# Kernel optimization log

Measured on AMD Instinct MI355X. Metric: run time of the kernel, lower is better.

The kernel has to match this reference:

```python
import jax, jax.numpy as jnp
import numpy as np

B, N, G = 16, 6000, 512
NUM_PAD_GT = 64  # zero-padded gt rows per image


def _make_boxes(key, shape):
    # sample two corner points and sort so (y1,x1) <= (y2,x2)
    r = jax.random.uniform(key, shape[:-1] + (4,), dtype=jnp.float32)
    lo = jnp.minimum(r[..., :2], r[..., 2:])
    hi = jnp.maximum(r[..., :2], r[..., 2:])
    return jnp.concatenate([lo, hi], axis=-1)


def setup_inputs() -> dict:
    key = jax.random.key(0)
    k1, k2, k3 = jax.random.split(key, 3)
    rois = _make_boxes(k1, (B, N, 4))
    gt_boxes = _make_boxes(k2, (B, G, 4))
    # zero-pad tail gt rows (remove_zero_padding signal)
    gt_boxes = gt_boxes.at[:, G - NUM_PAD_GT:, :].set(0.0)
    # ids in [-2, 18]: <0 crowd, ==0 padding, >0 real classes
    gt_ids = jax.random.randint(k3, (B, G), 0, 21, dtype=jnp.int64) - 2
    gt_ids = jnp.where(jnp.arange(G) >= G - NUM_PAD_GT, 0, gt_ids)
    return {"rois": rois, "gt_ids": gt_ids, "gt_boxes": gt_boxes}


def _pairwise_iou(boxes1, boxes2):
    # boxes1: [B,N,4], boxes2: [B,G,4] in (y1,x1,y2,x2) -> IoU [B,N,G]
    b1 = boxes1[:, :, None, :]  # [B,N,1,4]
    b2 = boxes2[:, None, :, :]  # [B,1,G,4]
    y1 = jnp.maximum(b1[..., 0], b2[..., 0])
    x1 = jnp.maximum(b1[..., 1], b2[..., 1])
    y2 = jnp.minimum(b1[..., 2], b2[..., 2])
    x2 = jnp.minimum(b1[..., 3], b2[..., 3])
    inter = jnp.maximum(y2 - y1, 0.0) * jnp.maximum(x2 - x1, 0.0)
    area1 = (b1[..., 2] - b1[..., 0]) * (b1[..., 3] - b1[..., 1])
    area2 = (b2[..., 2] - b2[..., 0]) * (b2[..., 3] - b2[..., 1])
    union = area1 + area2 - inter
    return inter / (union + 1e-8)


def reference(rois, gt_ids, gt_boxes):
    # remove_zero_padding -> validity masks (jit-friendly: mask instead of gather)
    valid_roi = jnp.sum(jnp.abs(rois), axis=-1) > 0.0      # [B,N]
    valid_gt = jnp.sum(jnp.abs(gt_boxes), axis=-1) > 0.0   # [B,G]
    crowd = valid_gt & (gt_ids < 0)                          # [B,G]
    non_crowd = valid_gt & (gt_ids > 0)                      # [B,G]

    iou = _pairwise_iou(rois, gt_boxes)                      # [B,N,G]
    # max IoU against non-crowd / crowd gt subsets (masked cols -> 0, IoU >= 0)
    iou_nc_max = jnp.max(jnp.where(non_crowd[:, None, :], iou, 0.0), axis=2)
    iou_c_max = jnp.max(jnp.where(crowd[:, None, :], iou, 0.0), axis=2)
    iou_nc_max = jnp.where(valid_roi, iou_nc_max, 0.0)       # [B,N]
    iou_c_max = jnp.where(valid_roi, iou_c_max, 0.0)

    positive_mask = valid_roi & (iou_nc_max >= 0.5)
    negative_mask = valid_roi & (iou_nc_max < 0.5) & (iou_c_max < 1e-3)

    iou_maxes = jnp.stack([iou_nc_max, iou_c_max], axis=1)   # [B,2,N]
    return iou_maxes, positive_mask, negative_mask
```

## Files before the change

### kernel.cpp

```cpp
#include <hip/hip_runtime.h>

#define BB 16
#define NN 6000
#define GG 512
#define WAVES 8
#define RPT 2
#define RPB (RPT * 64)

__device__ __forceinline__ int rfl(int v) { return __builtin_amdgcn_readfirstlane(v); }

__global__ __launch_bounds__(64 * WAVES, 8) void det_kernel(
    const float4* __restrict__ rois,
    const int*    __restrict__ gt_ids,
    const float4* __restrict__ gt_boxes,
    float*        __restrict__ out)
{
    __shared__ float4 s_box[GG];
    __shared__ float4 s_area4[GG / 4];
    __shared__ float  s_ncm[WAVES][RPB];
    __shared__ float  s_cm[WAVES][RPB];
    __shared__ int    s_wn[WAVES], s_wc[WAVES];
    float* s_area = (float*)s_area4;

    const int b    = blockIdx.y;
    const int tid  = threadIdx.x;
    const int wave = tid >> 6;
    const int lane = tid & 63;

    const int nbase = blockIdx.x * RPB;
    float4 r[RPT];
    float  rs[RPT];
    #pragma unroll
    for (int i = 0; i < RPT; ++i) {
        int n = nbase + i * 64 + lane;
        r[i] = (n < NN) ? rois[b * NN + n] : make_float4(0.f, 0.f, 0.f, 0.f);
    }
    const float4 box = gt_boxes[b * GG + tid];
    const int    id  = gt_ids[b * GG + tid];

    #pragma unroll
    for (int i = 0; i < RPT; ++i)
        rs[i] = (r[i].z - r[i].x) * (r[i].w - r[i].y) + 1e-8f;

    const float asum = fabsf(box.x) + fabsf(box.y) + fabsf(box.z) + fabsf(box.w);
    const bool pn = (asum > 0.0f) && (id > 0);
    const bool pc = (asum > 0.0f) && (id < 0);
    const unsigned long long mn = __ballot(pn);
    const unsigned long long mc = __ballot(pc);
    if (lane == 0) { s_wn[wave] = __popcll(mn); s_wc[wave] = __popcll(mc); }
    __syncthreads();

    int bn = 0, bc = 0, ncnt = 0, ccnt = 0;
    #pragma unroll
    for (int w = 0; w < WAVES; ++w) {
        int pw = s_wn[w], cw = s_wc[w];
        if (w < wave) { bn += pw; bc += cw; }
        ncnt += pw; ccnt += cw;
    }
    const int lo = GG - ccnt;
    int nc_eff = (ncnt + 3) & ~3;
    int lo_pad = lo & ~3;
    if (nc_eff > lo_pad) nc_eff = lo_pad;

    {
        const unsigned long long lt = (1ULL << lane) - 1ULL;
        if (pn) {
            int idx = bn + __popcll(mn & lt);
            s_box[idx]  = box;
            s_area[idx] = (box.z - box.x) * (box.w - box.y);
        }
        if (pc) {
            int idx = (GG - 1) - (bc + __popcll(mc & lt));
            s_box[idx]  = box;
            s_area[idx] = (box.z - box.x) * (box.w - box.y);
        }
        const float4 z = make_float4(0.f, 0.f, 0.f, 0.f);
        if (tid < 4) {
            int i = ncnt + tid;
            if (i < nc_eff) { s_box[i] = z; s_area[i] = 0.f; }
        } else if (tid < 8) {
            int i = lo_pad + (tid - 4);
            if (i < lo) { s_box[i] = z; s_area[i] = 0.f; }
        }
    }
    __syncthreads();

    auto tval = [](const float4& rr, float rsum, const float4& g4, float ga) -> float {
        float dy = fminf(rr.z, g4.z) - fmaxf(rr.x, g4.x);
        float dx = fminf(rr.w, g4.w) - fmaxf(rr.y, g4.y);
        float inter = fmaxf(fmaxf(dy, 0.f) * dx, 0.f);
        return inter * __builtin_amdgcn_rcpf(rsum + ga);
    };

    float anc[RPT] = {0.f, 0.f};
    float ac[RPT]  = {0.f, 0.f};

    auto run = [&](int q0, int q1, float* acc) {
        if (q0 >= q1) return;
        float4 nb0 = s_box[4 * q0 + 0];
        float4 nb1 = s_box[4 * q0 + 1];
        float4 nb2 = s_box[4 * q0 + 2];
        float4 nb3 = s_box[4 * q0 + 3];
        float4 na  = s_area4[q0];
        #pragma unroll 2
        for (int q = q0; q < q1; ++q) {
            const float4 cb0 = nb0, cb1 = nb1, cb2 = nb2, cb3 = nb3, ca = na;
            const int qn = (q + 1 < q1) ? q + 1 : q0;
            nb0 = s_box[4 * qn + 0];
            nb1 = s_box[4 * qn + 1];
            nb2 = s_box[4 * qn + 2];
            nb3 = s_box[4 * qn + 3];
            na  = s_area4[qn];
            #pragma unroll
            for (int i = 0; i < RPT; ++i) {
                float t0 = tval(r[i], rs[i], cb0, ca.x);
                float t1 = tval(r[i], rs[i], cb1, ca.y);
                float t2 = tval(r[i], rs[i], cb2, ca.z);
                float t3 = tval(r[i], rs[i], cb3, ca.w);
                acc[i] = fmaxf(acc[i], fmaxf(fmaxf(t0, t1), fmaxf(t2, t3)));
            }
        }
    };

    {
        const int ngr = nc_eff >> 2;
        const int gpw = (ngr + WAVES - 1) / WAVES;
        const int q0 = rfl(wave * gpw);
        const int q1 = rfl(min(ngr, q0 + gpw));
        run(q0, q1, anc);
    }
    {
        const int cg0 = lo_pad >> 2;
        const int cgn = (GG >> 2) - cg0;
        const int gpw = (cgn + WAVES - 1) / WAVES;
        const int q0 = rfl(cg0 + wave * gpw);
        const int q1 = rfl(min(GG >> 2, q0 + gpw));
        run(q0, q1, ac);
    }

    #pragma unroll
    for (int i = 0; i < RPT; ++i) {
        s_ncm[wave][i * 64 + lane] = anc[i];
        s_cm[wave][i * 64 + lane]  = ac[i];
    }
    __syncthreads();

    if (tid < RPB) {
        const int n = nbase + tid;
        if (n < NN) {
            float a = s_ncm[0][tid], c = s_cm[0][tid];
            #pragma unroll
            for (int w = 1; w < WAVES; ++w) {
                a = fmaxf(a, s_ncm[w][tid]);
                c = fmaxf(c, s_cm[w][tid]);
            }
            const float4 rr = (tid < 64) ? r[0] : r[1];
            const float vr =
                ((fabsf(rr.x) + fabsf(rr.y) + fabsf(rr.z) + fabsf(rr.w)) > 0.f) ? 1.f : 0.f;
            a *= vr;
            c *= vr;
            const float nc_max = a * __builtin_amdgcn_rcpf(1.f - a);
            const float c_max  = c * __builtin_amdgcn_rcpf(1.f - c);

            out[b * 2 * NN + n]      = nc_max;
            out[b * 2 * NN + NN + n] = c_max;
            const float pos = (vr > 0.f && nc_max >= 0.5f) ? 1.0f : 0.0f;
            const float neg = (vr > 0.f && nc_max < 0.5f && c_max < 0.001f) ? 1.0f : 0.0f;
            out[BB * 2 * NN + b * NN + n]           = pos;
            out[BB * 2 * NN + BB * NN + b * NN + n] = neg;
        }
    }
}

extern "C" void kernel_launch(void* const* d_in, const int* in_sizes, int n_in,
                              void* d_out, int out_size, void* d_ws, size_t ws_size,
                              hipStream_t stream) {
    const float4* rois     = (const float4*)d_in[0];
    const int*    gt_ids   = (const int*)d_in[1];
    const float4* gt_boxes = (const float4*)d_in[2];
    float*        out      = (float*)d_out;

    dim3 grid((NN + RPB - 1) / RPB, BB);
    det_kernel<<<grid, 64 * WAVES, 0, stream>>>(rois, gt_ids, gt_boxes, out);
}
```

Measured before the change: 25.08 us.

## Process three ROIs per lane with packed float2 math and inline gt areas

Raises the ROIs per thread from two to three, so each LDS-loaded gt box is reused across more ROIs and the grid shrinks. Two of the ROIs are computed with float2 operations, which may map to packed FP32 instructions, and the third is handled as a scalar. The separate gt area array in LDS is removed and each area is recomputed in the loop. ROI validity is staged through shared memory. The occupancy hint is dropped from launch bounds, so register pressure and occupancy can change, and with 6000 not divisible by 192 the last block has more idle lanes.

```diff
diff --git a/kernel.cpp b/kernel.cpp
--- a/kernel.cpp
+++ b/kernel.cpp
@@ -4,23 +4,24 @@
 #define NN 6000
 #define GG 512
 #define WAVES 8
-#define RPT 2
+#define RPT 3
 #define RPB (RPT * 64)
 
 __device__ __forceinline__ int rfl(int v) { return __builtin_amdgcn_readfirstlane(v); }
-
-__global__ __launch_bounds__(64 * WAVES, 8) void det_kernel(
+__device__ __forceinline__ float2 min2s(float2 a, float s) { return make_float2(fminf(a.x, s), fminf(a.y, s)); }
+__device__ __forceinline__ float2 max2s(float2 a, float s) { return make_float2(fmaxf(a.x, s), fmaxf(a.y, s)); }
+
+__global__ __launch_bounds__(64 * WAVES) void det_kernel(
     const float4* __restrict__ rois,
     const int*    __restrict__ gt_ids,
     const float4* __restrict__ gt_boxes,
     float*        __restrict__ out)
 {
     __shared__ float4 s_box[GG];
-    __shared__ float4 s_area4[GG / 4];
     __shared__ float  s_ncm[WAVES][RPB];
     __shared__ float  s_cm[WAVES][RPB];
+    __shared__ float  s_val[RPB];
     __shared__ int    s_wn[WAVES], s_wc[WAVES];
-    float* s_area = (float*)s_area4;
 
     const int b    = blockIdx.y;
     const int tid  = threadIdx.x;
@@ -29,7 +30,6 @@
 
     const int nbase = blockIdx.x * RPB;
     float4 r[RPT];
-    float  rs[RPT];
     #pragma unroll
     for (int i = 0; i < RPT; ++i) {
         int n = nbase + i * 64 + lane;
@@ -38,9 +38,14 @@
     const float4 box = gt_boxes[b * GG + tid];
     const int    id  = gt_ids[b * GG + tid];
 
+    float rsv[RPT];
     #pragma unroll
-    for (int i = 0; i < RPT; ++i)
-        rs[i] = (r[i].z - r[i].x) * (r[i].w - r[i].y) + 1e-8f;
+    for (int i = 0; i < RPT; ++i) {
+        rsv[i] = (r[i].z - r[i].x) * (r[i].w - r[i].y) + 1e-8f;
+        if (wave == 0)
+            s_val[i * 64 + lane] =
+                ((fabsf(r[i].x) + fabsf(r[i].y) + fabsf(r[i].z) + fabsf(r[i].w)) > 0.f) ? 1.f : 0.f;
+    }
 
     const float asum = fabsf(box.x) + fabsf(box.y) + fabsf(box.z) + fabsf(box.w);
     const bool pn = (asum > 0.0f) && (id > 0);
@@ -64,61 +69,74 @@
 
     {
         const unsigned long long lt = (1ULL << lane) - 1ULL;
-        if (pn) {
-            int idx = bn + __popcll(mn & lt);
-            s_box[idx]  = box;
-            s_area[idx] = (box.z - box.x) * (box.w - box.y);
-        }
-        if (pc) {
-            int idx = (GG - 1) - (bc + __popcll(mc & lt));
-            s_box[idx]  = box;
-            s_area[idx] = (box.z - box.x) * (box.w - box.y);
-        }
+        if (pn) s_box[bn + __popcll(mn & lt)] = box;
+        if (pc) s_box[(GG - 1) - (bc + __popcll(mc & lt))] = box;
         const float4 z = make_float4(0.f, 0.f, 0.f, 0.f);
         if (tid < 4) {
             int i = ncnt + tid;
-            if (i < nc_eff) { s_box[i] = z; s_area[i] = 0.f; }
+            if (i < nc_eff) s_box[i] = z;
         } else if (tid < 8) {
             int i = lo_pad + (tid - 4);
-            if (i < lo) { s_box[i] = z; s_area[i] = 0.f; }
+            if (i < lo) s_box[i] = z;
         }
     }
     __syncthreads();
 
-    auto tval = [](const float4& rr, float rsum, const float4& g4, float ga) -> float {
-        float dy = fminf(rr.z, g4.z) - fmaxf(rr.x, g4.x);
-        float dx = fminf(rr.w, g4.w) - fmaxf(rr.y, g4.y);
-        float inter = fmaxf(fmaxf(dy, 0.f) * dx, 0.f);
-        return inter * __builtin_amdgcn_rcpf(rsum + ga);
+    const float2 ry1c = make_float2(r[0].x, r[1].x);
+    const float2 rx1c = make_float2(r[0].y, r[1].y);
+    const float2 ry2c = make_float2(r[0].z, r[1].z);
+    const float2 rx2c = make_float2(r[0].w, r[1].w);
+    const float2 rs01 = make_float2(rsv[0], rsv[1]);
+    const float4 r2   = r[2];
+    const float  rs2  = rsv[2];
+
+    auto tduo = [&](const float4& g4, float ga) -> float2 {
+        float2 dy = min2s(ry2c, g4.z) - max2s(ry1c, g4.x);
+        float2 dx = min2s(rx2c, g4.w) - max2s(rx1c, g4.y);
+        float2 p  = max2s(dy, 0.f) * dx;
+        float2 it = max2s(p, 0.f);
+        return make_float2(it.x * __builtin_amdgcn_rcpf(rs01.x + ga),
+                           it.y * __builtin_amdgcn_rcpf(rs01.y + ga));
     };
-
-    float anc[RPT] = {0.f, 0.f};
-    float ac[RPT]  = {0.f, 0.f};
-
-    auto run = [&](int q0, int q1, float* acc) {
+    auto tsc = [&](const float4& g4, float ga) -> float {
+        float dy = fminf(r2.z, g4.z) - fmaxf(r2.x, g4.x);
+        float dx = fminf(r2.w, g4.w) - fmaxf(r2.y, g4.y);
+        float it = fmaxf(fmaxf(dy, 0.f) * dx, 0.f);
+        return it * __builtin_amdgcn_rcpf(rs2 + ga);
+    };
+
+    float2 a01n = make_float2(0.f, 0.f), a01c = make_float2(0.f, 0.f);
+    float  a2n = 0.f, a2c = 0.f;
+
+    auto run = [&](int q0, int q1, float2& acc2, float& acc1) {
         if (q0 >= q1) return;
         float4 nb0 = s_box[4 * q0 + 0];
         float4 nb1 = s_box[4 * q0 + 1];
         float4 nb2 = s_box[4 * q0 + 2];
         float4 nb3 = s_box[4 * q0 + 3];
-        float4 na  = s_area4[q0];
         #pragma unroll 2
         for (int q = q0; q < q1; ++q) {
-            const float4 cb0 = nb0, cb1 = nb1, cb2 = nb2, cb3 = nb3, ca = na;
+            const float4 cb0 = nb0, cb1 = nb1, cb2 = nb2, cb3 = nb3;
             const int qn = (q + 1 < q1) ? q + 1 : q0;
             nb0 = s_box[4 * qn + 0];
             nb1 = s_box[4 * qn + 1];
             nb2 = s_box[4 * qn + 2];
             nb3 = s_box[4 * qn + 3];
-            na  = s_area4[qn];
-            #pragma unroll
-            for (int i = 0; i < RPT; ++i) {
-                float t0 = tval(r[i], rs[i], cb0, ca.x);
-                float t1 = tval(r[i], rs[i], cb1, ca.y);
-                float t2 = tval(r[i], rs[i], cb2, ca.z);
-                float t3 = tval(r[i], rs[i], cb3, ca.w);
-                acc[i] = fmaxf(acc[i], fmaxf(fmaxf(t0, t1), fmaxf(t2, t3)));
-            }
+            const float ga0 = (cb0.z - cb0.x) * (cb0.w - cb0.y);
+            const float ga1 = (cb1.z - cb1.x) * (cb1.w - cb1.y);
+            const float ga2 = (cb2.z - cb2.x) * (cb2.w - cb2.y);
+            const float ga3 = (cb3.z - cb3.x) * (cb3.w - cb3.y);
+            float2 t0 = tduo(cb0, ga0);
+            float2 t1 = tduo(cb1, ga1);
+            float2 t2 = tduo(cb2, ga2);
+            float2 t3 = tduo(cb3, ga3);
+            acc2.x = fmaxf(fmaxf(fmaxf(fmaxf(t0.x, t1.x), t2.x), t3.x), acc2.x);
+            acc2.y = fmaxf(fmaxf(fmaxf(fmaxf(t0.y, t1.y), t2.y), t3.y), acc2.y);
+            float u0 = tsc(cb0, ga0);
+            float u1 = tsc(cb1, ga1);
+            float u2 = tsc(cb2, ga2);
+            float u3 = tsc(cb3, ga3);
+            acc1 = fmaxf(fmaxf(fmaxf(fmaxf(u0, u1), u2), u3), acc1);
         }
     };
 
@@ -127,7 +145,7 @@
         const int gpw = (ngr + WAVES - 1) / WAVES;
         const int q0 = rfl(wave * gpw);
         const int q1 = rfl(min(ngr, q0 + gpw));
-        run(q0, q1, anc);
+        run(q0, q1, a01n, a2n);
     }
     {
         const int cg0 = lo_pad >> 2;
@@ -135,14 +153,15 @@
         const int gpw = (cgn + WAVES - 1) / WAVES;
         const int q0 = rfl(cg0 + wave * gpw);
         const int q1 = rfl(min(GG >> 2, q0 + gpw));
-        run(q0, q1, ac);
-    }
-
-    #pragma unroll
-    for (int i = 0; i < RPT; ++i) {
-        s_ncm[wave][i * 64 + lane] = anc[i];
-        s_cm[wave][i * 64 + lane]  = ac[i];
-    }
+        run(q0, q1, a01c, a2c);
+    }
+
+    s_ncm[wave][lane]       = a01n.x;
+    s_ncm[wave][64 + lane]  = a01n.y;
+    s_ncm[wave][128 + lane] = a2n;
+    s_cm[wave][lane]        = a01c.x;
+    s_cm[wave][64 + lane]   = a01c.y;
+    s_cm[wave][128 + lane]  = a2c;
     __syncthreads();
 
     if (tid < RPB) {
@@ -154,9 +173,7 @@
                 a = fmaxf(a, s_ncm[w][tid]);
                 c = fmaxf(c, s_cm[w][tid]);
             }
-            const float4 rr = (tid < 64) ? r[0] : r[1];
-            const float vr =
-                ((fabsf(rr.x) + fabsf(rr.y) + fabsf(rr.z) + fabsf(rr.w)) > 0.f) ? 1.f : 0.f;
+            const float vr = s_val[tid];
             a *= vr;
             c *= vr;
             const float nc_max = a * __builtin_amdgcn_rcpf(1.f - a);
```

Result: faster. 24.16 us (-3.7%).
